# Kernel optimization log

Hardware: AMD Instinct MI355X
Metric: run time of the kernel (lower is better)

## Reference

```python
import jax, jax.numpy as jnp
import numpy as np

M, OUT, IN = 512, 8192, 8192
BLOCK_N, BLOCK_K = 128, 128  # weight_block_size (out_block, in_block)
OB, IB = OUT // BLOCK_N, IN // BLOCK_K  # 64, 64 scale blocks


def setup_inputs() -> dict:
    key = jax.random.key(0)
    k1, k2, k3 = jax.random.split(key, 3)
    x = jax.random.normal(k1, (M, IN), dtype=jnp.float32)
    # pre-quantized int8 weight stored as (out_features, in_features)
    weight_q = jax.random.randint(k2, (OUT, IN), -127, 127, dtype=jnp.int32).astype(jnp.int8)
    # per-(out_block, in_block) dequant scales
    weight_scale = jax.random.uniform(k3, (OB, IB), dtype=jnp.float32, minval=0.01, maxval=0.02)
    return {"x": x, "weight_q": weight_q, "weight_scale": weight_scale}


def _dequant(weight_q, weight_scale):
    # (OUT, IN) int8 -> blocks (OB, BLOCK_N, IB, BLOCK_K), scale broadcast per block
    w = weight_q.astype(jnp.float32).reshape(OB, BLOCK_N, IB, BLOCK_K)
    w = w * weight_scale[:, None, :, None]
    return w.reshape(OUT, IN)


def reference(x, weight_q, weight_scale):
    # Block-dequantize then matmul: out[m, o] = sum_i x[m, i] * (wq[o, i] * scale[o//bn, i//bk])
    w = _dequant(weight_q, weight_scale)          # (OUT, IN) fp32
    out = jnp.einsum("mi,oi->mo", x, w)           # (M, OUT)
    return out
```

## Files before the change

kernel.cpp:

```cpp
#include <hip/hip_runtime.h>

#define MDIM 512
#define NDIM 8192
#define KDIM 8192

typedef float v4f __attribute__((ext_vector_type(4)));
typedef int   v4i __attribute__((ext_vector_type(4)));
typedef char  c16 __attribute__((ext_vector_type(16)));

#define GLDS16(g, l)                                                    \
  __builtin_amdgcn_global_load_lds(                                     \
      (const __attribute__((address_space(1))) void*)(g),               \
      (__attribute__((address_space(3))) void*)(l), 16, 0, 0)
#define SB __builtin_amdgcn_sched_barrier(0)

__device__ __forceinline__ int swb(int row, int g) {
  return ((row >> 1) << 7) + (((((row & 1) << 2) | g) ^ ((row >> 1) & 7)) << 4);
}

__global__ __launch_bounds__(256) void produce_kernel(
    const int* __restrict__ wq, const float* __restrict__ x,
    char* __restrict__ w8, char* __restrict__ xq, float* __restrict__ ax) {
  if (blockIdx.x < 16384) {
    const int tid = blockIdx.x * 256 + threadIdx.x;
    const int R = tid >> 9;
    const int k16 = tid & 511;
    const int* src = wq + ((size_t)R << 13) + k16 * 16;
    v4i a[4];
#pragma unroll
    for (int h = 0; h < 4; ++h) a[h] = *(const v4i*)(src + h * 4);
    c16 q;
#pragma unroll
    for (int h = 0; h < 4; ++h) {
      q[h * 4 + 0] = (char)a[h][0];
      q[h * 4 + 1] = (char)a[h][1];
      q[h * 4 + 2] = (char)a[h][2];
      q[h * 4 + 3] = (char)a[h][3];
    }
    const int nt = R >> 6, r = R & 63;
    const int kt = k16 >> 2, g = k16 & 3;
    *(c16*)(w8 + ((size_t)(nt * 128 + kt) << 12) + swb(r, g)) = q;
  } else {
    const int m = blockIdx.x - 16384;
    const int t = threadIdx.x;
    const float* row = x + ((size_t)m << 13);
    v4f v[8];
    float mx = 0.f;
#pragma unroll
    for (int i = 0; i < 8; ++i) {
      v[i] = *(const v4f*)(row + t * 32 + i * 4);
#pragma unroll
      for (int r = 0; r < 4; ++r) mx = fmaxf(mx, fabsf(v[i][r]));
    }
#pragma unroll
    for (int d = 1; d < 64; d <<= 1) mx = fmaxf(mx, __shfl_xor(mx, d));
    __shared__ float smx[4];
    if ((t & 63) == 0) smx[t >> 6] = mx;
    __syncthreads();
    mx = fmaxf(fmaxf(smx[0], smx[1]), fmaxf(smx[2], smx[3]));
    const float inv = (mx > 0.f) ? 127.f / mx : 0.f;
    if (t == 0) ax[m] = mx / 127.f;
    const int mt = m >> 7, r = m & 127;
#pragma unroll
    for (int g2 = 0; g2 < 2; ++g2) {
      c16 q;
#pragma unroll
      for (int e = 0; e < 16; ++e) {
        const int idx = g2 * 4 + (e >> 2);
        float f = fminf(fmaxf(v[idx][e & 3] * inv, -127.f), 127.f);
        q[e] = (char)__float2int_rn(f);
      }
      const int k16 = t * 2 + g2;
      const int kt = k16 >> 2, g = k16 & 3;
      *(c16*)(xq + ((size_t)(mt * 128 + kt) << 13) + swb(r, g)) = q;
    }
  }
}

template <int KS>
__global__ __launch_bounds__(256) void reduce_kernel(const float* __restrict__ p,
                                                     float* __restrict__ out) {
  const size_t i = ((size_t)blockIdx.x * 256 + threadIdx.x) * 4;
  v4f a = *(const v4f*)(p + i);
#pragma unroll
  for (int s = 1; s < KS; ++s) a += *(const v4f*)(p + (size_t)s * MDIM * NDIM + i);
  *(v4f*)(out + i) = a;
}

template <int KS>
__global__ __launch_bounds__(512) void gemm_i8_kernel(
    const char* __restrict__ xq, const char* __restrict__ w8,
    const float* __restrict__ wsc, const float* __restrict__ ax,
    float* __restrict__ outp) {
  constexpr int NKT = 128 / KS;
  __shared__ char lA[2][8192];
  __shared__ char lB[2][8192];

  const int b = blockIdx.x;
  const int c = b & 7;
  const int s = b >> 3;
  const int mt = s & 3;
  const int kh = (KS > 1) ? ((s >> 2) & (KS - 1)) : 0;
  const int nt2 = c * 8 + ((KS > 1) ? (s >> 3) : (s >> 2));
  const int m0 = mt * 128, n0 = nt2 * 128;
  const int kt0 = kh * NKT;

  const int t = threadIdx.x;
  const int w = t >> 6, l = t & 63;
  const int wm = (w >> 2) * 64;
  const int wn = (w & 3) * 32;
  const int l15 = l & 15, q = l >> 4;

  const char* aS = xq + ((size_t)(mt * 128 + kt0) << 13) + (size_t)(w * 64 + l) * 16;
  const char* bS = w8 + ((size_t)((nt2 * 2 + (w >> 2)) * 128 + kt0) << 12) +
                   (size_t)((w & 3) * 64 + l) * 16;

  v4i acc[4][2] = {};
  v4f facc[4][2] = {};

  auto issue = [&](int tt) {
    const int buf = tt & 1;
    GLDS16(aS + ((size_t)tt << 13), &lA[buf][w * 1024]);
    GLDS16(bS + ((size_t)tt << 12), &lB[buf][w * 1024]);
  };

  issue(0);
#pragma unroll 1
  for (int tt = 0; tt < NKT; ++tt) {
    const int cur = tt & 1;
    SB;
    __builtin_amdgcn_s_barrier();
    SB;
    if (tt + 1 < NKT) issue(tt + 1);
    SB;
    if (tt + 1 < NKT)
      asm volatile("s_waitcnt vmcnt(2)" ::: "memory");
    else
      asm volatile("s_waitcnt vmcnt(0)" ::: "memory");
    SB;
    __builtin_amdgcn_s_barrier();
    SB;

    v4i af[4], bq[2];
#pragma unroll
    for (int i = 0; i < 4; ++i)
      af[i] = *(const v4i*)&lA[cur][swb(wm + i * 16 + l15, q)];
#pragma unroll
    for (int j = 0; j < 2; ++j) {
      const int rl = (wn & 63) + j * 16 + l15;
      bq[j] = *(const v4i*)&lB[cur][(wn >> 6) * 4096 + swb(rl, q)];
    }
#pragma unroll
    for (int i = 0; i < 4; ++i)
#pragma unroll
      for (int j = 0; j < 2; ++j)
        acc[i][j] = __builtin_amdgcn_mfma_i32_16x16x64_i8(
            af[i], bq[j], acc[i][j], 0, 0, 0);

    if (tt & 1) {
      const float sc = wsc[nt2 * 64 + ((kt0 + tt) >> 1)];
#pragma unroll
      for (int i = 0; i < 4; ++i)
#pragma unroll
        for (int j = 0; j < 2; ++j) {
#pragma unroll
          for (int r = 0; r < 4; ++r)
            facc[i][j][r] = fmaf(sc, (float)acc[i][j][r], facc[i][j][r]);
          acc[i][j] = v4i{0, 0, 0, 0};
        }
    }
  }

  float* dst = outp + ((KS > 1) ? (size_t)kh * MDIM * NDIM : 0);
#pragma unroll
  for (int i = 0; i < 4; ++i) {
    const int mrow = m0 + wm + i * 16 + (l >> 4) * 4;
#pragma unroll
    for (int j = 0; j < 2; ++j) {
      const int ocol = n0 + wn + j * 16 + l15;
#pragma unroll
      for (int r = 0; r < 4; ++r)
        dst[(size_t)(mrow + r) * NDIM + ocol] = ax[mrow + r] * facc[i][j][r];
    }
  }
}

extern "C" void kernel_launch(void* const* d_in, const int* in_sizes, int n_in,
                              void* d_out, int out_size, void* d_ws,
                              size_t ws_size, hipStream_t stream) {
  const float* x = (const float*)d_in[0];
  const int* wq = (const int*)d_in[1];
  const float* wsc = (const float*)d_in[2];
  float* out = (float*)d_out;

  const size_t W8 = (size_t)NDIM * KDIM;
  const size_t XQ = (size_t)MDIM * KDIM;
  const size_t AX = 65536;
  const size_t PS = (size_t)MDIM * NDIM * 4;

  char* w8 = (char*)d_ws;
  char* xq = (char*)d_ws + W8;
  float* ax = (float*)((char*)d_ws + W8 + XQ);
  float* part = (float*)((char*)d_ws + W8 + XQ + AX);

  produce_kernel<<<dim3(16384 + MDIM), dim3(256), 0, stream>>>(wq, x, w8, xq, ax);

  if (ws_size >= W8 + XQ + AX + 2 * PS) {
    gemm_i8_kernel<2><<<dim3(512), dim3(512), 0, stream>>>(xq, w8, wsc, ax, part);
    reduce_kernel<2><<<dim3((MDIM * NDIM) / (256 * 4)), dim3(256), 0, stream>>>(part, out);
  } else {
    gemm_i8_kernel<1><<<dim3(256), dim3(512), 0, stream>>>(xq, w8, wsc, ax, out);
  }
}
```

Baseline: 139.0 us.

## Use 4-wave blocks with 64x64 warp tiles and two k-tiles per stage

The GEMM block drops from 8 waves to 4, so each wave now computes a 64x64 output tile (4x4 MFMAs) instead of 64x32, which raises register-level reuse of the A and B fragments. Each pipeline stage now loads two 64-deep k-tiles (one full 128-wide scale block) into larger double-buffered LDS, with 8 async loads per wave. The x-quant layout changes to 64-row tiles to match, and the per-scale-block float rescale now runs once per stage. Register and LDS use per block go up (launch_bounds 256,2), which may limit occupancy.

Result: faster. 127.7 us (median of 2 runs) (-8.1%).

```diff
diff --git a/kernel.cpp b/kernel.cpp
--- a/kernel.cpp
+++ b/kernel.cpp
@@ -37,9 +37,9 @@
       q[h * 4 + 2] = (char)a[h][2];
       q[h * 4 + 3] = (char)a[h][3];
     }
-    const int nt = R >> 6, r = R & 63;
+    const int ntile = R >> 6, r = R & 63;
     const int kt = k16 >> 2, g = k16 & 3;
-    *(c16*)(w8 + ((size_t)(nt * 128 + kt) << 12) + swb(r, g)) = q;
+    *(c16*)(w8 + ((size_t)(ntile * 128 + kt) << 12) + swb(r, g)) = q;
   } else {
     const int m = blockIdx.x - 16384;
     const int t = threadIdx.x;
@@ -60,7 +60,7 @@
     mx = fmaxf(fmaxf(smx[0], smx[1]), fmaxf(smx[2], smx[3]));
     const float inv = (mx > 0.f) ? 127.f / mx : 0.f;
     if (t == 0) ax[m] = mx / 127.f;
-    const int mt = m >> 7, r = m & 127;
+    const int mt = m >> 6, r = m & 63;
 #pragma unroll
     for (int g2 = 0; g2 < 2; ++g2) {
       c16 q;
@@ -72,7 +72,7 @@
       }
       const int k16 = t * 2 + g2;
       const int kt = k16 >> 2, g = k16 & 3;
-      *(c16*)(xq + ((size_t)(mt * 128 + kt) << 13) + swb(r, g)) = q;
+      *(c16*)(xq + ((size_t)(mt * 128 + kt) << 12) + swb(r, g)) = q;
     }
   }
 }
@@ -88,13 +88,13 @@
 }
 
 template <int KS>
-__global__ __launch_bounds__(512) void gemm_i8_kernel(
+__global__ __launch_bounds__(256, 2) void gemm_i8_kernel(
     const char* __restrict__ xq, const char* __restrict__ w8,
     const float* __restrict__ wsc, const float* __restrict__ ax,
     float* __restrict__ outp) {
-  constexpr int NKT = 128 / KS;
-  __shared__ char lA[2][8192];
-  __shared__ char lB[2][8192];
+  constexpr int NPH = 64 / KS;
+  __shared__ char lA[2][16384];
+  __shared__ char lB[2][16384];
 
   const int b = blockIdx.x;
   const int c = b & 7;
@@ -102,82 +102,97 @@
   const int mt = s & 3;
   const int kh = (KS > 1) ? ((s >> 2) & (KS - 1)) : 0;
   const int nt2 = c * 8 + ((KS > 1) ? (s >> 3) : (s >> 2));
-  const int m0 = mt * 128, n0 = nt2 * 128;
-  const int kt0 = kh * NKT;
+  const int ktg0 = kh * (128 / KS);
 
   const int t = threadIdx.x;
   const int w = t >> 6, l = t & 63;
-  const int wm = (w >> 2) * 64;
-  const int wn = (w & 3) * 32;
+  const int wm = (w >> 1) * 64;
+  const int wn = (w & 1) * 64;
   const int l15 = l & 15, q = l >> 4;
 
-  const char* aS = xq + ((size_t)(mt * 128 + kt0) << 13) + (size_t)(w * 64 + l) * 16;
-  const char* bS = w8 + ((size_t)((nt2 * 2 + (w >> 2)) * 128 + kt0) << 12) +
-                   (size_t)((w & 3) * 64 + l) * 16;
-
-  v4i acc[4][2] = {};
-  v4f facc[4][2] = {};
+  v4i acc[4][4] = {};
+  v4f facc[4][4] = {};
 
   auto issue = [&](int tt) {
     const int buf = tt & 1;
-    GLDS16(aS + ((size_t)tt << 13), &lA[buf][w * 1024]);
-    GLDS16(bS + ((size_t)tt << 12), &lB[buf][w * 1024]);
+#pragma unroll
+    for (int it = 0; it < 8; ++it) {
+      const int uu = w * 8 + it;
+      const int side = uu >> 4;
+      const int h = (uu >> 3) & 1;
+      const int kt = (uu >> 2) & 1;
+      const int qt = uu & 3;
+      const int ktile = ktg0 + tt * 2 + kt;
+      const char* src =
+          (side == 0)
+              ? xq + ((size_t)((mt * 2 + h) * 128 + ktile) << 12)
+              : w8 + ((size_t)((nt2 * 2 + h) * 128 + ktile) << 12);
+      src += qt * 1024 + (size_t)l * 16;
+      char* dst = (side == 0) ? &lA[buf][h * 8192 + kt * 4096 + qt * 1024]
+                              : &lB[buf][h * 8192 + kt * 4096 + qt * 1024];
+      GLDS16(src, dst);
+    }
   };
 
   issue(0);
 #pragma unroll 1
-  for (int tt = 0; tt < NKT; ++tt) {
+  for (int tt = 0; tt < NPH; ++tt) {
     const int cur = tt & 1;
     SB;
     __builtin_amdgcn_s_barrier();
     SB;
-    if (tt + 1 < NKT) issue(tt + 1);
-    SB;
-    if (tt + 1 < NKT)
-      asm volatile("s_waitcnt vmcnt(2)" ::: "memory");
+    if (tt + 1 < NPH) issue(tt + 1);
+    SB;
+    if (tt + 1 < NPH)
+      asm volatile("s_waitcnt vmcnt(8)" ::: "memory");
     else
       asm volatile("s_waitcnt vmcnt(0)" ::: "memory");
     SB;
     __builtin_amdgcn_s_barrier();
     SB;
 
-    v4i af[4], bq[2];
+#pragma unroll
+    for (int kk = 0; kk < 2; ++kk) {
+      v4i af[4], bq[4];
+#pragma unroll
+      for (int i = 0; i < 4; ++i) {
+        const int ra = wm + i * 16 + l15;
+        af[i] = *(const v4i*)&lA[cur][(ra >> 6) * 8192 + kk * 4096 +
+                                      swb(ra & 63, q)];
+      }
+#pragma unroll
+      for (int j = 0; j < 4; ++j) {
+        const int rb = wn + j * 16 + l15;
+        bq[j] = *(const v4i*)&lB[cur][(rb >> 6) * 8192 + kk * 4096 +
+                                      swb(rb & 63, q)];
+      }
+#pragma unroll
+      for (int i = 0; i < 4; ++i)
+#pragma unroll
+        for (int j = 0; j < 4; ++j)
+          acc[i][j] = __builtin_amdgcn_mfma_i32_16x16x64_i8(
+              af[i], bq[j], acc[i][j], 0, 0, 0);
+    }
+
+    const float sc = wsc[nt2 * 64 + (ktg0 >> 1) + tt];
 #pragma unroll
     for (int i = 0; i < 4; ++i)
-      af[i] = *(const v4i*)&lA[cur][swb(wm + i * 16 + l15, q)];
-#pragma unroll
-    for (int j = 0; j < 2; ++j) {
-      const int rl = (wn & 63) + j * 16 + l15;
-      bq[j] = *(const v4i*)&lB[cur][(wn >> 6) * 4096 + swb(rl, q)];
-    }
-#pragma unroll
-    for (int i = 0; i < 4; ++i)
-#pragma unroll
-      for (int j = 0; j < 2; ++j)
-        acc[i][j] = __builtin_amdgcn_mfma_i32_16x16x64_i8(
-            af[i], bq[j], acc[i][j], 0, 0, 0);
-
-    if (tt & 1) {
-      const float sc = wsc[nt2 * 64 + ((kt0 + tt) >> 1)];
-#pragma unroll
-      for (int i = 0; i < 4; ++i)
-#pragma unroll
-        for (int j = 0; j < 2; ++j) {
-#pragma unroll
-          for (int r = 0; r < 4; ++r)
-            facc[i][j][r] = fmaf(sc, (float)acc[i][j][r], facc[i][j][r]);
-          acc[i][j] = v4i{0, 0, 0, 0};
-        }
-    }
+#pragma unroll
+      for (int j = 0; j < 4; ++j) {
+#pragma unroll
+        for (int r = 0; r < 4; ++r)
+          facc[i][j][r] = fmaf(sc, (float)acc[i][j][r], facc[i][j][r]);
+        acc[i][j] = v4i{0, 0, 0, 0};
+      }
   }
 
   float* dst = outp + ((KS > 1) ? (size_t)kh * MDIM * NDIM : 0);
 #pragma unroll
   for (int i = 0; i < 4; ++i) {
-    const int mrow = m0 + wm + i * 16 + (l >> 4) * 4;
-#pragma unroll
-    for (int j = 0; j < 2; ++j) {
-      const int ocol = n0 + wn + j * 16 + l15;
+    const int mrow = mt * 128 + wm + i * 16 + q * 4;
+#pragma unroll
+    for (int j = 0; j < 4; ++j) {
+      const int ocol = nt2 * 128 + wn + j * 16 + l15;
 #pragma unroll
       for (int r = 0; r < 4; ++r)
         dst[(size_t)(mrow + r) * NDIM + ocol] = ax[mrow + r] * facc[i][j][r];
@@ -206,9 +221,9 @@
   produce_kernel<<<dim3(16384 + MDIM), dim3(256), 0, stream>>>(wq, x, w8, xq, ax);
 
   if (ws_size >= W8 + XQ + AX + 2 * PS) {
-    gemm_i8_kernel<2><<<dim3(512), dim3(512), 0, stream>>>(xq, w8, wsc, ax, part);
+    gemm_i8_kernel<2><<<dim3(512), dim3(256), 0, stream>>>(xq, w8, wsc, ax, part);
     reduce_kernel<2><<<dim3((MDIM * NDIM) / (256 * 4)), dim3(256), 0, stream>>>(part, out);
   } else {
-    gemm_i8_kernel<1><<<dim3(256), dim3(512), 0, stream>>>(xq, w8, wsc, ax, out);
-  }
-}
+    gemm_i8_kernel<1><<<dim3(256), dim3(256), 0, stream>>>(xq, w8, wsc, ax, out);
+  }
+}
```
